# Optimization experiments

Hardware: AMD Instinct MI355X
Metric: run time of the kernel (lower is better)

The kernel has to match this reference:

```python
import jax, jax.numpy as jnp
import numpy as np

# Grid of blocks: blocks[i][j] is Linear(D, D) if mask[i, j] else None.
N_OUT, N_IN, D, B = 8, 8, 128, 32768
BAND = 2  # active blocks: j <= i and i - j <= BAND


def setup_inputs() -> dict:
    key = jax.random.key(0)
    k1, k2, k3 = jax.random.split(key, 3)
    # X: (num input blocks, batch, block feature dim)
    X = jax.random.normal(k1, (N_IN, B, D), dtype=jnp.float32)
    # W[i, j]: torch.nn.Linear weight of block (i, j), shape (out, in)
    W = jax.random.normal(k2, (N_OUT, N_IN, D, D), dtype=jnp.float32) / np.sqrt(D).astype(np.float32)
    b = jax.random.normal(k3, (N_OUT, N_IN, D), dtype=jnp.float32) * 0.01
    i = jnp.arange(N_OUT)[:, None]
    j = jnp.arange(N_IN)[None, :]
    mask = (j <= i) & (i - j <= BAND)  # banded lower-triangular block sparsity
    return {"X": X, "W": W, "b": b, "mask": mask}


def reference(X, W, b, mask):
    # Sequential2D forward: out[i] = sum_j (X[j] @ W[i,j].T + b[i,j]) over active blocks.
    # None blocks contribute a zero vector, which we express by zeroing masked weights/biases.
    m = mask.astype(W.dtype)                       # (i, j)
    Wm = W * m[:, :, None, None]                   # zero out None blocks
    out = jnp.einsum('jbd,ijod->ibo', X, Wm)       # block-row summation of Linear outputs
    bias = jnp.sum(b * m[:, :, None], axis=1)      # (i, o): sum of active biases per row
    return out + bias[:, None, :]                  # (num_out_blocks, batch, block_out)
```

## Files before the change

kernel.cpp:

```cpp
#include <hip/hip_runtime.h>
#include <hip/hip_bf16.h>


#define NOUT  8
#define NIN   8
#define DD    128
#define BATCH 32768
#define BAND  2

#define BM 128
#define BN 128
#define BK 64
#define SK (BK + 8)

typedef __attribute__((ext_vector_type(8))) short  short8;
typedef __attribute__((ext_vector_type(4))) float  floatx4;

__device__ __forceinline__ unsigned short f2bf(float f) {
    unsigned int u = __float_as_uint(f);
    u += 0x7fffu + ((u >> 16) & 1u);
    return (unsigned short)(u >> 16);
}

__global__ __launch_bounds__(256)
void seq2d_kernel(const float* __restrict__ X,
                  const float* __restrict__ W,
                  const float* __restrict__ Bv,
                  float* __restrict__ out) {
    const int i  = blockIdx.y;
    const int m0 = blockIdx.x * BM;

    __shared__ unsigned short sA[BM * SK];
    __shared__ unsigned short sB[BN * SK];
    __shared__ float sbias[DD];

    const int tid  = threadIdx.x;
    const int lane = tid & 63;
    const int wave = tid >> 6;
    const int wm   = (wave & 1) * 64;
    const int wn   = (wave >> 1) * 64;
    const int l15  = lane & 15;
    const int quad = lane >> 4;

    int jlo = i - BAND; if (jlo < 0) jlo = 0;

    if (tid < DD) {
        float s = 0.f;
        for (int j = jlo; j <= i; ++j)
            s += Bv[(i * NIN + j) * DD + tid];
        sbias[tid] = s;
    }

    floatx4 acc[4][4];
#pragma unroll
    for (int a = 0; a < 4; ++a)
#pragma unroll
        for (int c = 0; c < 4; ++c)
            acc[a][c] = (floatx4){0.f, 0.f, 0.f, 0.f};

    const int srow = tid >> 3;
    const int scol = (tid & 7) << 3;

    for (int j = jlo; j <= i; ++j) {
        const float* __restrict__ Xj  = X + (size_t)j * BATCH * DD;
        const float* __restrict__ Wij = W + (size_t)(i * NIN + j) * DD * DD;
#pragma unroll
        for (int k0 = 0; k0 < DD; k0 += BK) {
            __syncthreads();
#pragma unroll
            for (int rr = 0; rr < BM; rr += 32) {
                const float* src = Xj + (size_t)(m0 + rr + srow) * DD + (k0 + scol);
                floatx4 f0 = *(const floatx4*)(src);
                floatx4 f1 = *(const floatx4*)(src + 4);
                short8 p;
                p[0] = (short)f2bf(f0[0]); p[1] = (short)f2bf(f0[1]);
                p[2] = (short)f2bf(f0[2]); p[3] = (short)f2bf(f0[3]);
                p[4] = (short)f2bf(f1[0]); p[5] = (short)f2bf(f1[1]);
                p[6] = (short)f2bf(f1[2]); p[7] = (short)f2bf(f1[3]);
                *(short8*)(&sA[(rr + srow) * SK + scol]) = p;
            }
#pragma unroll
            for (int rr = 0; rr < BN; rr += 32) {
                const float* src = Wij + (size_t)(rr + srow) * DD + (k0 + scol);
                floatx4 f0 = *(const floatx4*)(src);
                floatx4 f1 = *(const floatx4*)(src + 4);
                short8 p;
                p[0] = (short)f2bf(f0[0]); p[1] = (short)f2bf(f0[1]);
                p[2] = (short)f2bf(f0[2]); p[3] = (short)f2bf(f0[3]);
                p[4] = (short)f2bf(f1[0]); p[5] = (short)f2bf(f1[1]);
                p[6] = (short)f2bf(f1[2]); p[7] = (short)f2bf(f1[3]);
                *(short8*)(&sB[(rr + srow) * SK + scol]) = p;
            }
            __syncthreads();
#pragma unroll
            for (int kk = 0; kk < BK; kk += 32) {
                short8 af[4], bf[4];
#pragma unroll
                for (int t = 0; t < 4; ++t) {
                    af[t] = *(const short8*)(&sA[(wm + t * 16 + l15) * SK + kk + quad * 8]);
                    bf[t] = *(const short8*)(&sB[(wn + t * 16 + l15) * SK + kk + quad * 8]);
                }
#pragma unroll
                for (int mt = 0; mt < 4; ++mt)
#pragma unroll
                    for (int nt = 0; nt < 4; ++nt)
                        acc[mt][nt] = __builtin_amdgcn_mfma_f32_16x16x32_bf16(
                            af[mt], bf[nt], acc[mt][nt], 0, 0, 0);
            }
        }
    }

    float* outi = out + (size_t)i * BATCH * DD;
#pragma unroll
    for (int mt = 0; mt < 4; ++mt) {
#pragma unroll
        for (int nt = 0; nt < 4; ++nt) {
            const int n_g  = wn + nt * 16 + l15;
            const float bs = sbias[n_g];
            const int m_b  = m0 + wm + mt * 16 + quad * 4;
#pragma unroll
            for (int r = 0; r < 4; ++r)
                outi[(size_t)(m_b + r) * DD + n_g] = acc[mt][nt][r] + bs;
        }
    }
}

extern "C" void kernel_launch(void* const* d_in, const int* in_sizes, int n_in,
                              void* d_out, int out_size, void* d_ws, size_t ws_size,
                              hipStream_t stream) {
    const float* X  = (const float*)d_in[0];
    const float* W  = (const float*)d_in[1];
    const float* Bv = (const float*)d_in[2];
    float* out = (float*)d_out;

    dim3 grid(BATCH / BM, NOUT);
    seq2d_kernel<<<grid, 256, 0, stream>>>(X, W, Bv, out);
}
```

Before: 276.3 us.

## Double the block to 512 threads and prefetch next K-chunk into registers

Moves the block from 4 to 8 waves, each owning a 64x32 output tile instead of 64x64, so there are more waves to hide latency. The j and k loops are flattened into one chunk loop, and the global loads for the next chunk are issued into registers while the current chunk is being computed. The aim is to overlap global memory latency with MFMA work. In exchange, each wave reuses its A fragments across fewer MFMAs, and the larger block may lower occupancy.

```diff
diff --git a/kernel.cpp b/kernel.cpp
--- a/kernel.cpp
+++ b/kernel.cpp
@@ -22,7 +22,16 @@
     return (unsigned short)(u >> 16);
 }
 
-__global__ __launch_bounds__(256)
+__device__ __forceinline__ short8 pack8(floatx4 f0, floatx4 f1) {
+    short8 p;
+    p[0] = (short)f2bf(f0[0]); p[1] = (short)f2bf(f0[1]);
+    p[2] = (short)f2bf(f0[2]); p[3] = (short)f2bf(f0[3]);
+    p[4] = (short)f2bf(f1[0]); p[5] = (short)f2bf(f1[1]);
+    p[6] = (short)f2bf(f1[2]); p[7] = (short)f2bf(f1[3]);
+    return p;
+}
+
+__global__ __launch_bounds__(512)
 void seq2d_kernel(const float* __restrict__ X,
                   const float* __restrict__ W,
                   const float* __restrict__ Bv,
@@ -38,11 +47,12 @@
     const int lane = tid & 63;
     const int wave = tid >> 6;
     const int wm   = (wave & 1) * 64;
-    const int wn   = (wave >> 1) * 64;
+    const int wn   = (wave >> 1) * 32;
     const int l15  = lane & 15;
     const int quad = lane >> 4;
 
     int jlo = i - BAND; if (jlo < 0) jlo = 0;
+    const int nc = (i - jlo + 1) * 2;
 
     if (tid < DD) {
         float s = 0.f;
@@ -51,62 +61,61 @@
         sbias[tid] = s;
     }
 
-    floatx4 acc[4][4];
+    floatx4 acc[4][2];
 #pragma unroll
     for (int a = 0; a < 4; ++a)
 #pragma unroll
-        for (int c = 0; c < 4; ++c)
+        for (int c = 0; c < 2; ++c)
             acc[a][c] = (floatx4){0.f, 0.f, 0.f, 0.f};
 
     const int srow = tid >> 3;
     const int scol = (tid & 7) << 3;
 
-    for (int j = jlo; j <= i; ++j) {
-        const float* __restrict__ Xj  = X + (size_t)j * BATCH * DD;
-        const float* __restrict__ Wij = W + (size_t)(i * NIN + j) * DD * DD;
+    floatx4 pa[4], pb[4];
+
+    auto prefetch = [&](int c) {
+        const int j  = jlo + (c >> 1);
+        const int k0 = (c & 1) * BK;
+        const float* __restrict__ xa =
+            X + (size_t)j * BATCH * DD + (size_t)(m0 + srow) * DD + k0 + scol;
+        pa[0] = *(const floatx4*)(xa);
+        pa[1] = *(const floatx4*)(xa + 4);
+        pa[2] = *(const floatx4*)(xa + 64 * DD);
+        pa[3] = *(const floatx4*)(xa + 64 * DD + 4);
+        const float* __restrict__ wb =
+            W + (size_t)(i * NIN + j) * DD * DD + (size_t)srow * DD + k0 + scol;
+        pb[0] = *(const floatx4*)(wb);
+        pb[1] = *(const floatx4*)(wb + 4);
+        pb[2] = *(const floatx4*)(wb + 64 * DD);
+        pb[3] = *(const floatx4*)(wb + 64 * DD + 4);
+    };
+
+    prefetch(0);
+
+    for (int c = 0; c < nc; ++c) {
+        __syncthreads();
+        *(short8*)(&sA[srow * SK + scol])        = pack8(pa[0], pa[1]);
+        *(short8*)(&sA[(64 + srow) * SK + scol]) = pack8(pa[2], pa[3]);
+        *(short8*)(&sB[srow * SK + scol])        = pack8(pb[0], pb[1]);
+        *(short8*)(&sB[(64 + srow) * SK + scol]) = pack8(pb[2], pb[3]);
+        if (c + 1 < nc) prefetch(c + 1);
+        __syncthreads();
+
 #pragma unroll
-        for (int k0 = 0; k0 < DD; k0 += BK) {
-            __syncthreads();
+        for (int kk = 0; kk < BK; kk += 32) {
+            short8 af[4], bfr[2];
 #pragma unroll
-            for (int rr = 0; rr < BM; rr += 32) {
-                const float* src = Xj + (size_t)(m0 + rr + srow) * DD + (k0 + scol);
-                floatx4 f0 = *(const floatx4*)(src);
-                floatx4 f1 = *(const floatx4*)(src + 4);
-                short8 p;
-                p[0] = (short)f2bf(f0[0]); p[1] = (short)f2bf(f0[1]);
-                p[2] = (short)f2bf(f0[2]); p[3] = (short)f2bf(f0[3]);
-                p[4] = (short)f2bf(f1[0]); p[5] = (short)f2bf(f1[1]);
-                p[6] = (short)f2bf(f1[2]); p[7] = (short)f2bf(f1[3]);
-                *(short8*)(&sA[(rr + srow) * SK + scol]) = p;
-            }
+            for (int t = 0; t < 4; ++t)
+                af[t] = *(const short8*)(&sA[(wm + t * 16 + l15) * SK + kk + quad * 8]);
 #pragma unroll
-            for (int rr = 0; rr < BN; rr += 32) {
-                const float* src = Wij + (size_t)(rr + srow) * DD + (k0 + scol);
-                floatx4 f0 = *(const floatx4*)(src);
-                floatx4 f1 = *(const floatx4*)(src + 4);
-                short8 p;
-                p[0] = (short)f2bf(f0[0]); p[1] = (short)f2bf(f0[1]);
-                p[2] = (short)f2bf(f0[2]); p[3] = (short)f2bf(f0[3]);
-                p[4] = (short)f2bf(f1[0]); p[5] = (short)f2bf(f1[1]);
-                p[6] = (short)f2bf(f1[2]); p[7] = (short)f2bf(f1[3]);
-                *(short8*)(&sB[(rr + srow) * SK + scol]) = p;
-            }
-            __syncthreads();
+            for (int t = 0; t < 2; ++t)
+                bfr[t] = *(const short8*)(&sB[(wn + t * 16 + l15) * SK + kk + quad * 8]);
 #pragma unroll
-            for (int kk = 0; kk < BK; kk += 32) {
-                short8 af[4], bf[4];
+            for (int mt = 0; mt < 4; ++mt)
 #pragma unroll
-                for (int t = 0; t < 4; ++t) {
-                    af[t] = *(const short8*)(&sA[(wm + t * 16 + l15) * SK + kk + quad * 8]);
-                    bf[t] = *(const short8*)(&sB[(wn + t * 16 + l15) * SK + kk + quad * 8]);
-                }
-#pragma unroll
-                for (int mt = 0; mt < 4; ++mt)
-#pragma unroll
-                    for (int nt = 0; nt < 4; ++nt)
-                        acc[mt][nt] = __builtin_amdgcn_mfma_f32_16x16x32_bf16(
-                            af[mt], bf[nt], acc[mt][nt], 0, 0, 0);
-            }
+                for (int nt = 0; nt < 2; ++nt)
+                    acc[mt][nt] = __builtin_amdgcn_mfma_f32_16x16x32_bf16(
+                        af[mt], bfr[nt], acc[mt][nt], 0, 0, 0);
         }
     }
 
@@ -114,7 +123,7 @@
 #pragma unroll
     for (int mt = 0; mt < 4; ++mt) {
 #pragma unroll
-        for (int nt = 0; nt < 4; ++nt) {
+        for (int nt = 0; nt < 2; ++nt) {
             const int n_g  = wn + nt * 16 + l15;
             const float bs = sbias[n_g];
             const int m_b  = m0 + wm + mt * 16 + quad * 4;
@@ -134,5 +143,5 @@
     float* out = (float*)d_out;
 
     dim3 grid(BATCH / BM, NOUT);
-    seq2d_kernel<<<grid, 256, 0, stream>>>(X, W, Bv, out);
+    seq2d_kernel<<<grid, 512, 0, stream>>>(X, W, Bv, out);
 }
```

Result: faster. 262.3 us (-5.1%).
